# Kernel optimization log

Measured on AMD Instinct MI355X. Metric: run time of the kernel, lower is better.

## Reference

```python
import jax, jax.numpy as jnp
import numpy as np


def log_g(x):
    # log of g(x) = where(x>=0, x+0.5, sigmoid(x))
    return jnp.where(x >= 0, jnp.log(jax.nn.relu(x) + 0.5), -jax.nn.softplus(-x))


def mingru_layer(x, h0, w, b):
    # x: (B,S,In), h0: (B,1,H), w: (2H,In), b: (2H,)
    B, S, _ = x.shape
    gh = jnp.einsum('bsi,oi->bso', x, w) + b          # (B,S,2H)
    H = gh.shape[-1] // 2
    gate, hidden = gh[..., :H], gh[..., H:]
    log_z = -jax.nn.softplus(-gate)                    # log sigmoid(gate)
    log_coeffs = -jax.nn.softplus(gate)                # log(1 - z)
    log_tilde_h = log_g(hidden)
    log_values = jnp.concatenate([jnp.log(h0), log_z + log_tilde_h], axis=1)  # (B,S+1,H)
    a_star = jnp.concatenate(
        [jnp.zeros((B, 1, H), dtype=x.dtype), jnp.cumsum(log_coeffs, axis=1)], axis=1
    )                                                  # (B,S+1,H)
    log_h = a_star + jax.lax.cumlogsumexp(log_values - a_star, axis=1)
    return jnp.exp(log_h)[:, 1:]                       # (B,S,H)


def setup_inputs() -> dict:
    key = jax.random.key(0)
    k = jax.random.split(key, 5)
    B, S, D, H = 8, 4096, 512, 512
    sc = 1.0 / np.sqrt(D)
    return {
        'x': jax.random.normal(k[0], (B, S, D), jnp.float32),
        'w0': jax.random.normal(k[1], (2 * H, D), jnp.float32) * sc,
        'b0': jax.random.normal(k[2], (2 * H,), jnp.float32) * 0.01,
        'w1': jax.random.normal(k[3], (2 * H, H), jnp.float32) * sc,
        'b1': jax.random.normal(k[4], (2 * H,), jnp.float32) * 0.01,
    }


def reference(x, w0, b0, w1, b1):
    B = x.shape[0]
    # init_hidden_state: g(zeros) = 0.5
    next_hidden = []
    inp = x
    for (w, b) in ((w0, b0), (w1, b1)):
        H = w.shape[0] // 2
        h0 = jnp.full((B, 1, H), 0.5, dtype=x.dtype)
        out = mingru_layer(inp, h0, w, b)
        next_hidden.append(out[:, -1:])
        inp = out
    return (out, jnp.stack(next_hidden))  # (B,S,H), (L,B,1,H)
```

## Files before the change

### kernel.cpp

```cpp
#include <hip/hip_runtime.h>
#include <math.h>


typedef unsigned short u16;
typedef __attribute__((ext_vector_type(8))) short short8;
typedef __attribute__((ext_vector_type(4))) float f32x4;

__device__ __forceinline__ u16 f2bf(float f) {
    unsigned int u = __float_as_uint(f);
    return (u16)((u + 0x7fffu + ((u >> 16) & 1u)) >> 16);
}
__device__ __forceinline__ float bf2f(u16 u) {
    return __uint_as_float(((unsigned int)u) << 16);
}
__device__ __forceinline__ void async16(const void* g, void* l) {
    __builtin_amdgcn_global_load_lds(
        (const __attribute__((address_space(1))) unsigned int*)g,
        (__attribute__((address_space(3))) unsigned int*)l, 16, 0, 0);
}

__device__ __forceinline__ void coeff_val(float gate, float hid, float& c, float& v)
{
    float eg  = __expf(-fabsf(gate));
    float inv = 1.0f / (1.0f + eg);
    float sp  = inv;
    float sn  = eg * inv;
    float z   = (gate >= 0.f) ? sp : sn;
    c         = (gate >= 0.f) ? sn : sp;
    float eh  = __expf(-fabsf(hid));
    float gneg = eh / (1.0f + eh);
    float g   = (hid >= 0.f) ? (hid + 0.5f) : gneg;
    v = z * g;
}

__global__ __launch_bounds__(256) void cast3(
    const float* __restrict__ x,  u16* __restrict__ xb,  int nx4,
    const float* __restrict__ w0, u16* __restrict__ w0b,
    const float* __restrict__ w1, u16* __restrict__ w1b, int nw4)
{
    int i = blockIdx.x * 256 + threadIdx.x;
    const float* src; u16* dst; int idx;
    if (i < nx4)                { src = x;  dst = xb;  idx = i; }
    else if (i < nx4 + nw4)     { src = w0; dst = w0b; idx = i - nx4; }
    else if (i < nx4 + 2 * nw4) { src = w1; dst = w1b; idx = i - nx4 - nw4; }
    else return;
    float4 v = ((const float4*)src)[idx];
    ushort4 o = make_ushort4(f2bf(v.x), f2bf(v.y), f2bf(v.z), f2bf(v.w));
    ((ushort4*)dst)[idx] = o;
}

#define TSTR 136

__global__ __launch_bounds__(256) void gemm_fused(
    const u16* __restrict__ A, const u16* __restrict__ W,
    const float* __restrict__ bias, u16* __restrict__ gh,
    float* __restrict__ cA, float* __restrict__ cV, int K)
{
    __shared__ __align__(16) u16 lds[128 * TSTR];
    __shared__ float2 csum[2][2][64];

    u16* Asm = lds;
    u16* Wsm = lds + 4096;

    const int tid  = threadIdx.x;
    const int bm   = blockIdx.y;
    const int bn   = blockIdx.x;
    const int lane = tid & 63;
    const int wave = tid >> 6;
    const int wm   = (wave >> 1) * 64;
    const int wn   = (wave & 1) * 64;
    const int fm   = lane & 15;
    const int kb   = lane >> 4;

    const int g0 = tid, g1 = tid + 256;
    const int r0 = g0 >> 2, q0 = (g0 & 3) ^ ((g0 >> 3) & 3);
    const int r1 = g1 >> 2, q1 = (g1 & 3) ^ ((g1 >> 3) & 3);
    const int wr0 = bn * 64 + (r0 & 63) + ((r0 >> 6) << 9);
    const int wr1 = bn * 64 + (r1 & 63) + ((r1 >> 6) << 9);
    const u16* Ap0 = A + (size_t)(bm * 128 + r0) * K + q0 * 8;
    const u16* Ap1 = A + (size_t)(bm * 128 + r1) * K + q1 * 8;
    const u16* Wp0 = W + (size_t)wr0 * K + q0 * 8;
    const u16* Wp1 = W + (size_t)wr1 * K + q1 * 8;
    char* lA0 = (char*)Asm + g0 * 16;
    char* lA1 = (char*)Asm + g1 * 16;
    char* lW0 = (char*)Wsm + g0 * 16;
    char* lW1 = (char*)Wsm + g1 * 16;

    int offA[4], offB[4];
    #pragma unroll
    for (int i = 0; i < 4; ++i) {
        int rowA = wm + i * 16 + fm;
        offA[i] = rowA * 64 + ((kb ^ ((rowA >> 1) & 3)) * 16);
        int rowB = wn + i * 16 + fm;
        offB[i] = rowB * 64 + ((kb ^ ((rowB >> 1) & 3)) * 16);
    }

    f32x4 acc[4][4];
    #pragma unroll
    for (int i = 0; i < 4; ++i)
        #pragma unroll
        for (int j = 0; j < 4; ++j)
            acc[i][j] = (f32x4){0.f, 0.f, 0.f, 0.f};

    const char* AsB = (const char*)Asm;
    const char* WsB = (const char*)Wsm;

    for (int kt = 0; kt < K; kt += 32) {
        async16(Ap0, lA0);
        async16(Ap1, lA1);
        async16(Wp0, lW0);
        async16(Wp1, lW1);
        __syncthreads();
        short8 a[4], b[4];
        #pragma unroll
        for (int i = 0; i < 4; ++i) a[i] = *(const short8*)(AsB + offA[i]);
        #pragma unroll
        for (int j = 0; j < 4; ++j) b[j] = *(const short8*)(WsB + offB[j]);
        #pragma unroll
        for (int i = 0; i < 4; ++i)
            #pragma unroll
            for (int j = 0; j < 4; ++j)
                acc[i][j] = __builtin_amdgcn_mfma_f32_16x16x32_bf16(
                    a[i], b[j], acc[i][j], 0, 0, 0);
        __syncthreads();
        Ap0 += 32; Ap1 += 32; Wp0 += 32; Wp1 += 32;
    }

    float bv[4];
    #pragma unroll
    for (int j = 0; j < 4; ++j) {
        int c = wn + j * 16 + fm;
        bv[j] = bias[bn * 64 + (c & 63) + ((c >> 6) << 9)];
    }
    #pragma unroll
    for (int i = 0; i < 4; ++i)
        #pragma unroll
        for (int j = 0; j < 4; ++j) {
            const int col = wn + j * 16 + fm;
            f32x4 v = acc[i][j];
            #pragma unroll
            for (int r = 0; r < 4; ++r)
                lds[(wm + i * 16 + kb * 4 + r) * TSTR + col] = f2bf(v[r] + bv[j]);
        }
    __syncthreads();

    #pragma unroll
    for (int it = 0; it < 8; ++it) {
        const int h   = it & 1;
        const int row = (it >> 1) * 32 + (tid >> 3);
        const int sc  = (tid & 7) * 8;
        short8 vv = *(const short8*)&lds[row * TSTR + h * 64 + sc];
        *(short8*)&gh[(size_t)(bm * 128 + row) * 1024 + h * 512 + bn * 64 + sc] = vv;
    }

    const int ch   = tid & 63;
    const int half = (tid >> 6) & 1;
    const int ck   = tid >> 7;
    float Aa = 1.f, Vv = 0.f;
    const int rbase = ck * 64 + half * 32;
    #pragma unroll 4
    for (int s = 0; s < 32; ++s) {
        const int row = rbase + s;
        float gate = bf2f(lds[row * TSTR + ch]);
        float hid  = bf2f(lds[row * TSTR + 64 + ch]);
        float c, v; coeff_val(gate, hid, c, v);
        Aa *= c;
        Vv = fmaf(c, Vv, v);
    }
    csum[ck][half][ch] = make_float2(Aa, Vv);
    __syncthreads();
    if (half == 0) {
        float2 s0 = csum[ck][0][ch];
        float2 s1 = csum[ck][1][ch];
        float Ac = s1.x * s0.x;
        float Vc = fmaf(s1.x, s0.y, s1.y);
        const int b   = bm >> 5;
        const int ckg = (bm & 31) * 2 + ck;
        const size_t idx = ((size_t)(b * 64 + ckg)) * 512 + bn * 64 + ch;
        cA[idx] = Ac;
        cV[idx] = Vc;
    }
}

__global__ __launch_bounds__(256) void scan_pass2(
    const float* __restrict__ cA, const float* __restrict__ cV,
    float* __restrict__ carry, int Nc)
{
    const int tid = threadIdx.x;
    const int b = blockIdx.x;
    float s0 = 0.5f, s1 = 0.5f;
    #pragma unroll 8
    for (int ck = 0; ck < Nc; ++ck) {
        const size_t idx = (size_t)(b * Nc + ck) * 512 + 2 * tid;
        *(float2*)(carry + idx) = make_float2(s0, s1);
        float2 a = *(const float2*)(cA + idx);
        float2 v = *(const float2*)(cV + idx);
        s0 = fmaf(a.x, s0, v.x);
        s1 = fmaf(a.y, s1, v.y);
    }
}

template <bool OUT_BF16>
__global__ __launch_bounds__(256) void scan_pass3(
    const u16* __restrict__ gh, const float* __restrict__ carry,
    void* __restrict__ outv, float* __restrict__ nh,
    int S, int Lc, int Nc)
{
    const int tid = threadIdx.x;
    const int b  = blockIdx.x / Nc;
    const int ck = blockIdx.x % Nc;
    const u16* base = gh + (size_t)(b * S + ck * Lc) * 1024 + 2 * tid;
    const size_t cidx = (size_t)(b * Nc + ck) * 512 + 2 * tid;
    float2 st = *(const float2*)(carry + cidx);
    float h0 = st.x, h1 = st.y;
    const size_t obase = (size_t)(b * S + ck * Lc) * 512 + 2 * tid;
    #pragma unroll 4
    for (int s = 0; s < Lc; ++s) {
        ushort2 g2 = *(const ushort2*)(base + (size_t)s * 1024);
        ushort2 h2 = *(const ushort2*)(base + (size_t)s * 1024 + 512);
        float c0, v0, c1, v1;
        coeff_val(bf2f(g2.x), bf2f(h2.x), c0, v0);
        coeff_val(bf2f(g2.y), bf2f(h2.y), c1, v1);
        h0 = fmaf(c0, h0, v0);
        h1 = fmaf(c1, h1, v1);
        if (OUT_BF16) {
            ushort2 o = make_ushort2(f2bf(h0), f2bf(h1));
            *(ushort2*)((u16*)outv + obase + (size_t)s * 512) = o;
        } else {
            *(float2*)((float*)outv + obase + (size_t)s * 512) = make_float2(h0, h1);
        }
    }
    if (ck == Nc - 1)
        *(float2*)(nh + (size_t)b * 512 + 2 * tid) = make_float2(h0, h1);
}

extern "C" void kernel_launch(void* const* d_in, const int* in_sizes, int n_in,
                              void* d_out, int out_size, void* d_ws, size_t ws_size,
                              hipStream_t stream)
{
    const float* x  = (const float*)d_in[0];
    const float* w0 = (const float*)d_in[1];
    const float* b0 = (const float*)d_in[2];
    const float* w1 = (const float*)d_in[3];
    const float* b1 = (const float*)d_in[4];
    float* out = (float*)d_out;

    const int B = 8, S = 4096, K = 512;
    const int M = B * S;
    const int Lc = 64, Nc = S / Lc;

    u16* gh  = (u16*)d_ws;
    u16* xb  = gh  + (size_t)M * 1024;
    u16* h0b = xb  + (size_t)M * 512;
    u16* w0b = h0b + (size_t)M * 512;
    u16* w1b = w0b + (size_t)1024 * 512;
    float* cA    = (float*)(w1b + (size_t)1024 * 512);
    float* cV    = cA + (size_t)B * Nc * 512;
    float* carry = cV + (size_t)B * Nc * 512;

    float* nh0 = out + (size_t)M * 512;
    float* nh1 = nh0 + (size_t)B * 512;

    dim3 blk(256);
    dim3 ggrid(8, M / 128);
    dim3 sgrid(B * Nc);

    const int nx4 = M * K / 4;
    const int nw4 = 1024 * K / 4;
    cast3<<<dim3((nx4 + 2 * nw4 + 255) / 256), blk, 0, stream>>>(
        x, xb, nx4, w0, w0b, w1, w1b, nw4);

    gemm_fused<<<ggrid, blk, 0, stream>>>(xb, w0b, b0, gh, cA, cV, K);
    scan_pass2<<<dim3(B), blk, 0, stream>>>(cA, cV, carry, Nc);
    scan_pass3<true><<<sgrid, blk, 0, stream>>>(gh, carry, h0b, nh0, S, Lc, Nc);

    gemm_fused<<<ggrid, blk, 0, stream>>>(h0b, w1b, b1, gh, cA, cV, K);
    scan_pass2<<<dim3(B), blk, 0, stream>>>(cA, cV, carry, Nc);
    scan_pass3<false><<<sgrid, blk, 0, stream>>>(gh, carry, out, nh1, S, Lc, Nc);
}
```

Measured before the change: 323.0 us.

## Store precomputed coefficient/value pairs from GEMM epilogue and deepen K tile

The GEMM epilogue now evaluates the gate and hidden nonlinearities once and writes interleaved bf16 (coefficient, value) pairs instead of raw gate/hidden pre-activations. The scan pass then needs only one fused multiply-add per element, with no transcendental work. The K tile doubles to 64 with an 8-way LDS swizzle, block indices are remapped across the grid, and coeff_val switches to a hardware reciprocal. The risks are lower accuracy from rounding the coefficient to bf16 before it is multiplied along the scan, and from the approximate reciprocal.

```diff
diff --git a/kernel.cpp b/kernel.cpp
--- a/kernel.cpp
+++ b/kernel.cpp
@@ -18,19 +18,16 @@
         (const __attribute__((address_space(1))) unsigned int*)g,
         (__attribute__((address_space(3))) unsigned int*)l, 16, 0, 0);
 }
+__device__ __forceinline__ float fastrcp(float x) { return __builtin_amdgcn_rcpf(x); }
 
 __device__ __forceinline__ void coeff_val(float gate, float hid, float& c, float& v)
 {
-    float eg  = __expf(-fabsf(gate));
-    float inv = 1.0f / (1.0f + eg);
-    float sp  = inv;
-    float sn  = eg * inv;
-    float z   = (gate >= 0.f) ? sp : sn;
-    c         = (gate >= 0.f) ? sn : sp;
-    float eh  = __expf(-fabsf(hid));
-    float gneg = eh / (1.0f + eh);
-    float g   = (hid >= 0.f) ? (hid + 0.5f) : gneg;
-    v = z * g;
+    float cc = fastrcp(1.0f + __expf(gate));
+    float gp = hid + 0.5f;
+    float gn = fastrcp(1.0f + __expf(-hid));
+    float g  = (hid >= 0.0f) ? gp : gn;
+    c = cc;
+    v = (1.0f - cc) * g;
 }
 
 __global__ __launch_bounds__(256) void cast3(
@@ -49,50 +46,53 @@
     ((ushort4*)dst)[idx] = o;
 }
 
-#define TSTR 136
+#define TST 144
 
 __global__ __launch_bounds__(256) void gemm_fused(
     const u16* __restrict__ A, const u16* __restrict__ W,
     const float* __restrict__ bias, u16* __restrict__ gh,
     float* __restrict__ cA, float* __restrict__ cV, int K)
 {
-    __shared__ __align__(16) u16 lds[128 * TSTR];
+    __shared__ __align__(16) u16 lds[128 * TST];
     __shared__ float2 csum[2][2][64];
 
     u16* Asm = lds;
-    u16* Wsm = lds + 4096;
+    u16* Wsm = lds + 8192;
 
     const int tid  = threadIdx.x;
-    const int bm   = blockIdx.y;
-    const int bn   = blockIdx.x;
+    const int d    = blockIdx.y * 8 + blockIdx.x;
+    const int cpx  = (int)(gridDim.x * gridDim.y) >> 3;
+    const int t0   = (d & 7) * cpx + (d >> 3);
+    const int bn   = t0 & 7;
+    const int bm   = t0 >> 3;
     const int lane = tid & 63;
     const int wave = tid >> 6;
     const int wm   = (wave >> 1) * 64;
     const int wn   = (wave & 1) * 64;
+    const int w1   = wave & 1;
     const int fm   = lane & 15;
     const int kb   = lane >> 4;
 
-    const int g0 = tid, g1 = tid + 256;
-    const int r0 = g0 >> 2, q0 = (g0 & 3) ^ ((g0 >> 3) & 3);
-    const int r1 = g1 >> 2, q1 = (g1 & 3) ^ ((g1 >> 3) & 3);
-    const int wr0 = bn * 64 + (r0 & 63) + ((r0 >> 6) << 9);
-    const int wr1 = bn * 64 + (r1 & 63) + ((r1 >> 6) << 9);
-    const u16* Ap0 = A + (size_t)(bm * 128 + r0) * K + q0 * 8;
-    const u16* Ap1 = A + (size_t)(bm * 128 + r1) * K + q1 * 8;
-    const u16* Wp0 = W + (size_t)wr0 * K + q0 * 8;
-    const u16* Wp1 = W + (size_t)wr1 * K + q1 * 8;
-    char* lA0 = (char*)Asm + g0 * 16;
-    char* lA1 = (char*)Asm + g1 * 16;
-    char* lW0 = (char*)Wsm + g0 * 16;
-    char* lW1 = (char*)Wsm + g1 * 16;
+    const u16* Ap[4]; const u16* Wp[4]; char* lA[4]; char* lW[4];
+    #pragma unroll
+    for (int t = 0; t < 4; ++t) {
+        const int gt = tid + 256 * t;
+        const int r  = gt >> 3;
+        const int q  = (gt & 7) ^ (r & 7);
+        Ap[t] = A + (size_t)(bm * 128 + r) * K + q * 8;
+        const int wr = bn * 64 + (r & 31) + ((r & 64) >> 1) + ((r & 32) ? 512 : 0);
+        Wp[t] = W + (size_t)wr * K + q * 8;
+        lA[t] = (char*)Asm + gt * 16;
+        lW[t] = (char*)Wsm + gt * 16;
+    }
 
     int offA[4], offB[4];
     #pragma unroll
     for (int i = 0; i < 4; ++i) {
-        int rowA = wm + i * 16 + fm;
-        offA[i] = rowA * 64 + ((kb ^ ((rowA >> 1) & 3)) * 16);
-        int rowB = wn + i * 16 + fm;
-        offB[i] = rowB * 64 + ((kb ^ ((rowB >> 1) & 3)) * 16);
+        const int rowA = wm + i * 16 + fm;
+        offA[i] = rowA * 128 + ((kb ^ (rowA & 7)) * 16);
+        const int rowB = wn + i * 16 + fm;
+        offB[i] = rowB * 128 + ((kb ^ (rowB & 7)) * 16);
     }
 
     f32x4 acc[4][4];
@@ -105,52 +105,62 @@
     const char* AsB = (const char*)Asm;
     const char* WsB = (const char*)Wsm;
 
-    for (int kt = 0; kt < K; kt += 32) {
-        async16(Ap0, lA0);
-        async16(Ap1, lA1);
-        async16(Wp0, lW0);
-        async16(Wp1, lW1);
+    for (int kt = 0; kt < K; kt += 64) {
+        #pragma unroll
+        for (int t = 0; t < 4; ++t) { async16(Ap[t], lA[t]); async16(Wp[t], lW[t]); }
         __syncthreads();
-        short8 a[4], b[4];
-        #pragma unroll
-        for (int i = 0; i < 4; ++i) a[i] = *(const short8*)(AsB + offA[i]);
-        #pragma unroll
-        for (int j = 0; j < 4; ++j) b[j] = *(const short8*)(WsB + offB[j]);
-        #pragma unroll
-        for (int i = 0; i < 4; ++i)
-            #pragma unroll
-            for (int j = 0; j < 4; ++j)
-                acc[i][j] = __builtin_amdgcn_mfma_f32_16x16x32_bf16(
-                    a[i], b[j], acc[i][j], 0, 0, 0);
+        #pragma unroll
+        for (int ks = 0; ks < 2; ++ks) {
+            const int xo = ks << 6;
+            short8 a[4], b[4];
+            #pragma unroll
+            for (int i = 0; i < 4; ++i) a[i] = *(const short8*)(AsB + (offA[i] ^ xo));
+            #pragma unroll
+            for (int j = 0; j < 4; ++j) b[j] = *(const short8*)(WsB + (offB[j] ^ xo));
+            #pragma unroll
+            for (int i = 0; i < 4; ++i)
+                #pragma unroll
+                for (int j = 0; j < 4; ++j)
+                    acc[i][j] = __builtin_amdgcn_mfma_f32_16x16x32_bf16(
+                        a[i], b[j], acc[i][j], 0, 0, 0);
+        }
         __syncthreads();
-        Ap0 += 32; Ap1 += 32; Wp0 += 32; Wp1 += 32;
-    }
-
-    float bv[4];
-    #pragma unroll
-    for (int j = 0; j < 4; ++j) {
-        int c = wn + j * 16 + fm;
-        bv[j] = bias[bn * 64 + (c & 63) + ((c >> 6) << 9)];
-    }
+        #pragma unroll
+        for (int t = 0; t < 4; ++t) { Ap[t] += 64; Wp[t] += 64; }
+    }
+
+    float bg[2], bh[2];
+    #pragma unroll
+    for (int jj = 0; jj < 2; ++jj) {
+        const int chl = w1 * 32 + jj * 16 + fm;
+        bg[jj] = bias[bn * 64 + chl];
+        bh[jj] = bias[512 + bn * 64 + chl];
+    }
+    unsigned int* ldsw = (unsigned int*)lds;
     #pragma unroll
     for (int i = 0; i < 4; ++i)
         #pragma unroll
-        for (int j = 0; j < 4; ++j) {
-            const int col = wn + j * 16 + fm;
-            f32x4 v = acc[i][j];
-            #pragma unroll
-            for (int r = 0; r < 4; ++r)
-                lds[(wm + i * 16 + kb * 4 + r) * TSTR + col] = f2bf(v[r] + bv[j]);
+        for (int jj = 0; jj < 2; ++jj) {
+            const int chl = w1 * 32 + jj * 16 + fm;
+            const f32x4 g4 = acc[i][jj];
+            const f32x4 h4 = acc[i][jj + 2];
+            #pragma unroll
+            for (int r = 0; r < 4; ++r) {
+                const int row = wm + i * 16 + kb * 4 + r;
+                float c, v;
+                coeff_val(g4[r] + bg[jj], h4[r] + bh[jj], c, v);
+                ldsw[row * 72 + chl] = (unsigned int)f2bf(c)
+                                     | ((unsigned int)f2bf(v) << 16);
+            }
         }
     __syncthreads();
 
     #pragma unroll
     for (int it = 0; it < 8; ++it) {
-        const int h   = it & 1;
-        const int row = (it >> 1) * 32 + (tid >> 3);
-        const int sc  = (tid & 7) * 8;
-        short8 vv = *(const short8*)&lds[row * TSTR + h * 64 + sc];
-        *(short8*)&gh[(size_t)(bm * 128 + row) * 1024 + h * 512 + bn * 64 + sc] = vv;
+        const int row = it * 16 + (tid >> 4);
+        const int sc  = (tid & 15) * 8;
+        short8 vv = *(const short8*)&lds[row * TST + sc];
+        *(short8*)&gh[(size_t)(bm * 128 + row) * 1024 + bn * 128 + sc] = vv;
     }
 
     const int ch   = tid & 63;
@@ -160,10 +170,9 @@
     const int rbase = ck * 64 + half * 32;
     #pragma unroll 4
     for (int s = 0; s < 32; ++s) {
-        const int row = rbase + s;
-        float gate = bf2f(lds[row * TSTR + ch]);
-        float hid  = bf2f(lds[row * TSTR + 64 + ch]);
-        float c, v; coeff_val(gate, hid, c, v);
+        const unsigned int p = ldsw[(rbase + s) * 72 + ch];
+        const float c = bf2f((u16)p);
+        const float v = bf2f((u16)(p >> 16));
         Aa *= c;
         Vv = fmaf(c, Vv, v);
     }
@@ -209,20 +218,16 @@
     const int tid = threadIdx.x;
     const int b  = blockIdx.x / Nc;
     const int ck = blockIdx.x % Nc;
-    const u16* base = gh + (size_t)(b * S + ck * Lc) * 1024 + 2 * tid;
+    const u16* base = gh + (size_t)(b * S + ck * Lc) * 1024 + 4 * tid;
     const size_t cidx = (size_t)(b * Nc + ck) * 512 + 2 * tid;
     float2 st = *(const float2*)(carry + cidx);
     float h0 = st.x, h1 = st.y;
     const size_t obase = (size_t)(b * S + ck * Lc) * 512 + 2 * tid;
     #pragma unroll 4
     for (int s = 0; s < Lc; ++s) {
-        ushort2 g2 = *(const ushort2*)(base + (size_t)s * 1024);
-        ushort2 h2 = *(const ushort2*)(base + (size_t)s * 1024 + 512);
-        float c0, v0, c1, v1;
-        coeff_val(bf2f(g2.x), bf2f(h2.x), c0, v0);
-        coeff_val(bf2f(g2.y), bf2f(h2.y), c1, v1);
-        h0 = fmaf(c0, h0, v0);
-        h1 = fmaf(c1, h1, v1);
+        ushort4 q = *(const ushort4*)(base + (size_t)s * 1024);
+        h0 = fmaf(bf2f(q.x), h0, bf2f(q.y));
+        h1 = fmaf(bf2f(q.z), h1, bf2f(q.w));
         if (OUT_BF16) {
             ushort2 o = make_ushort2(f2bf(h0), f2bf(h1));
             *(ushort2*)((u16*)outv + obase + (size_t)s * 512) = o;
```

New measurement: 273.9 us. -15.2%, faster.
